# Kernel optimization log

Hardware: AMD Instinct MI355X
Metric: run time of the kernel (lower is better)

Reference implementation:

```python
import jax, jax.numpy as jnp
import numpy as np

NMS_PRE_MAXSIZE = 4096
NMS_POST_MAXSIZE = 512
NMS_THRESH = 0.7


def setup_inputs() -> dict:
    key = jax.random.key(0)
    k1, k2, k3, k4, k5 = jax.random.split(key, 5)
    B, N, C = 4, 32768, 3
    # realistic 3D boxes: (x, y, z, dx, dy, dz, heading)
    xy = jax.random.uniform(k1, (B, N, 2), dtype=jnp.float32) * 70.0
    z = jax.random.uniform(k2, (B, N, 1), dtype=jnp.float32) * 4.0 - 2.0
    sizes = jax.random.uniform(k3, (B, N, 3), dtype=jnp.float32) * 3.0 + 1.0
    heading = jax.random.uniform(k4, (B, N, 1), dtype=jnp.float32) * 6.2832 - 3.1416
    batch_box_preds = jnp.concatenate([xy, z, sizes, heading], axis=-1)  # (B,N,7)
    batch_cls_preds = jax.random.uniform(k5, (B, N, C), dtype=jnp.float32)  # (B,N,3)
    return {"batch_box_preds": batch_box_preds, "batch_cls_preds": batch_cls_preds}


def _nms_single(boxes, scores, labels):
    # boxes (N,7), scores (N,), labels (N,) int32
    top_s, idx = jax.lax.top_k(scores, NMS_PRE_MAXSIZE)   # sort desc, keep pre-maxsize
    b = boxes[idx]                                        # (PRE,7)
    l = labels[idx]
    # BEV axis-aligned IoU (reference surrogate for the rotated-BEV CUDA IoU kernel)
    x, y, dx, dy = b[:, 0], b[:, 1], b[:, 3], b[:, 4]
    x1, x2 = x - 0.5 * dx, x + 0.5 * dx
    y1, y2 = y - 0.5 * dy, y + 0.5 * dy
    area = dx * dy
    ix = jnp.maximum(0.0, jnp.minimum(x2[:, None], x2[None, :]) - jnp.maximum(x1[:, None], x1[None, :]))
    iy = jnp.maximum(0.0, jnp.minimum(y2[:, None], y2[None, :]) - jnp.maximum(y1[:, None], y1[None, :]))
    inter = ix * iy
    iou = jax.lax.stop_gradient(inter / (area[:, None] + area[None, :] - inter + 1e-6))

    ar = jnp.arange(NMS_PRE_MAXSIZE)

    def body(i, keep):
        sup = (iou[i] > NMS_THRESH) & (ar > i) & keep[i]
        return keep & ~sup

    keep = jax.lax.fori_loop(0, NMS_PRE_MAXSIZE, body, jnp.ones(NMS_PRE_MAXSIZE, bool))

    # pack first NMS_POST_MAXSIZE kept boxes into fixed-size zero-padded outputs
    rank = jnp.cumsum(keep) - 1
    valid = keep & (rank < NMS_POST_MAXSIZE)
    pos = jnp.where(valid, rank, NMS_POST_MAXSIZE)  # invalid -> scratch row
    rois = jnp.zeros((NMS_POST_MAXSIZE + 1, 7), b.dtype).at[pos].set(b)[:NMS_POST_MAXSIZE]
    sc = jnp.zeros((NMS_POST_MAXSIZE + 1,), top_s.dtype).at[pos].set(top_s)[:NMS_POST_MAXSIZE]
    lb = jnp.zeros((NMS_POST_MAXSIZE + 1,), jnp.int32).at[pos].set(l)[:NMS_POST_MAXSIZE]
    return rois, sc, lb


def reference(batch_box_preds, batch_cls_preds):
    # per-box max score / argmax class (torch.max(cls_preds, dim=1) per sample)
    roi_scores_all = jnp.max(batch_cls_preds, axis=-1)                 # (B,N)
    roi_labels_all = jnp.argmax(batch_cls_preds, axis=-1).astype(jnp.int32)
    rois, roi_scores, roi_labels = jax.vmap(_nms_single)(batch_box_preds, roi_scores_all, roi_labels_all)
    return rois, roi_scores, roi_labels + 1  # labels shifted by +1 as in proposal_layer
```

## Files before the change

### kernel.cpp

```cpp
#include <hip/hip_runtime.h>
#include <stdint.h>

#define BB 4
#define NN 32768
#define PRE 4096
#define POST 512
#define NMS_TH 0.7f
#define MIDCAP 8192
#define NWAVE 16
#define KCAP 576

typedef unsigned long long u64;
typedef unsigned int u32;

__device__ __forceinline__ u32 orderable(float f) {
  u32 u = __float_as_uint(f);
  return (u & 0x80000000u) ? ~u : (u | 0x80000000u);
}
__device__ __forceinline__ float unorderable(u32 o) {
  u32 u = (o & 0x80000000u) ? (o & 0x7fffffffu) : ~o;
  return __uint_as_float(u);
}
__device__ __forceinline__ u32 bucket_of(float s) {
  u32 v = (u32)(s * 2147483648.0f);
  u32 bk = v >> 20;
  return bk > 2047u ? 2047u : bk;
}
__device__ __forceinline__ u64 readlane64(u64 v, int l) {
  u32 lo = (u32)__builtin_amdgcn_readlane((int)(u32)v, l);
  u32 hi = (u32)__builtin_amdgcn_readlane((int)(u32)(v >> 32), l);
  return ((u64)hi << 32) | lo;
}
__device__ __forceinline__ bool iou_fast(float4 a, float aa, float4 b, float ba, float& mm) {
  float ix = fminf(a.z, b.z) - fmaxf(a.x, b.x); ix = fmaxf(0.0f, ix);
  float iy = fminf(a.w, b.w) - fmaxf(a.y, b.y); iy = fmaxf(0.0f, iy);
  float inter = ix * iy;
  float denom = ((aa + ba) - inter) + 1e-6f;
  float t = 0.7f * denom;
  mm = fminf(mm, fabsf(inter - t) - 2e-5f * t);
  return inter > t;
}
__device__ __forceinline__ bool iou_exact(float4 a, float aa, float4 b, float ba) {
  float ix = fminf(a.z, b.z) - fmaxf(a.x, b.x); ix = fmaxf(0.0f, ix);
  float iy = fminf(a.w, b.w) - fmaxf(a.y, b.y); iy = fmaxf(0.0f, iy);
  float inter = ix * iy;
  float denom = ((aa + ba) - inter) + 1e-6f;
  return (inter / denom) > NMS_TH;
}

__global__ __launch_bounds__(1024, 1) void nms_all_kernel(
    const float* __restrict__ boxes, const float* __restrict__ cls,
    u64* __restrict__ keysG, int* __restrict__ labelsG,
    u64* __restrict__ selG, u64* __restrict__ midG,
    float4* __restrict__ Pg, float* __restrict__ ARg,
    float* __restrict__ topBox, float* __restrict__ topS, int* __restrict__ topL,
    float* __restrict__ out) {
  __shared__ u32 sfx[2048];
  __shared__ u32 cursor[2048];
  __shared__ float4 keptP[KCAP];
  __shared__ float keptAR[KCAP];
  __shared__ u64 dLDS[64];
  __shared__ u64 kwLDS[64];
  __shared__ u32 supArr[64];
  __shared__ u32 midCnt, Tsh, C1sh, knSh;

  int b = blockIdx.x;
  int tid = threadIdx.x;
  int wv = tid >> 6, lane = tid & 63;

  if (tid == 0) { midCnt = 0; knSh = 0; }
  if (tid < 64) kwLDS[tid] = 0;
  for (int t = tid; t < 2048; t += 1024) sfx[t] = 0;
  __syncthreads();

  u64* keysB = keysG + (size_t)b * NN;
  int* labsB = labelsG + (size_t)b * NN;
  const float* clsB = cls + (size_t)b * NN * 3;
  for (int c = 0; c < 8; ++c) {
    int t4 = tid + c * 1024;
    const float4* c4 = (const float4*)(clsB + (size_t)t4 * 12);
    float4 va = c4[0], vb = c4[1], vc = c4[2];
    float v[12] = {va.x, va.y, va.z, va.w, vb.x, vb.y, vb.z, vb.w, vc.x, vc.y, vc.z, vc.w};
    u64 ks[4]; int ls[4];
#pragma unroll
    for (int p = 0; p < 4; ++p) {
      float s = v[3 * p]; int l = 0;
      if (v[3 * p + 1] > s) { s = v[3 * p + 1]; l = 1; }
      if (v[3 * p + 2] > s) { s = v[3 * p + 2]; l = 2; }
      int n = t4 * 4 + p;
      ks[p] = ((u64)orderable(s) << 32) | (u32)(~(u32)n);
      ls[p] = l;
      atomicAdd(&sfx[bucket_of(s)], 1u);
    }
    *(ulonglong2*)(keysB + t4 * 4) = make_ulonglong2(ks[0], ks[1]);
    *(ulonglong2*)(keysB + t4 * 4 + 2) = make_ulonglong2(ks[2], ks[3]);
    *(int4*)(labsB + t4 * 4) = make_int4(ls[0], ls[1], ls[2], ls[3]);
  }
  __syncthreads();

  for (int d = 1; d < 2048; d <<= 1) {
    int t0 = tid, t1 = tid + 1024;
    u32 v0 = (t0 + d < 2048) ? sfx[t0 + d] : 0;
    u32 v1 = (t1 + d < 2048) ? sfx[t1 + d] : 0;
    __syncthreads();
    sfx[t0] += v0; sfx[t1] += v1;
    __syncthreads();
  }
#pragma unroll
  for (int i = 0; i < 2; ++i) {
    int t = tid + i * 1024;
    u32 above = (t + 1 < 2048) ? sfx[t + 1] : 0;
    cursor[t] = above;
    if (above < PRE && sfx[t] >= PRE) { Tsh = (u32)t; C1sh = above; }
  }
  __syncthreads();
  u32 T = Tsh, C1 = C1sh;

  u64* selB = selG + ((size_t)b << 12);
  u64* midB = midG + (size_t)b * MIDCAP;
  for (int c = 0; c < 8; ++c) {
    int t4 = tid + c * 1024;
    ulonglong2 k01 = *(const ulonglong2*)(keysB + t4 * 4);
    ulonglong2 k23 = *(const ulonglong2*)(keysB + t4 * 4 + 2);
    u64 kk[4] = {k01.x, k01.y, k23.x, k23.y};
#pragma unroll
    for (int p = 0; p < 4; ++p) {
      u64 key = kk[p];
      u32 bk = bucket_of(unorderable((u32)(key >> 32)));
      if (bk > T) {
        u32 q = atomicAdd(&cursor[bk], 1u);
        selB[q] = key;
      } else if (bk == T) {
        u32 q = atomicAdd(&midCnt, 1u);
        if (q < MIDCAP) midB[q] = key;
      }
    }
  }
  __syncthreads();

  for (int t = (int)T + wv; t < 2048; t += NWAVE) {
    if (t == (int)T) {
      int need = PRE - (int)C1;
      int M = (int)midCnt; if (M > MIDCAP) M = MIDCAP;
      for (int r = 0; r < need; ++r) {
        u64 best = 0; int bi = -1;
        for (int q = lane; q < M; q += 64) {
          u64 v = midB[q];
          if (v > best) { best = v; bi = q; }
        }
#pragma unroll
        for (int d = 32; d > 0; d >>= 1) {
          u64 ob = __shfl_xor(best, d, 64);
          int oi = __shfl_xor(bi, d, 64);
          if (ob > best) { best = ob; bi = oi; }
        }
        if (lane == 0) selB[C1 + r] = best;
        if (bi >= 0 && lane == (bi & 63)) midB[bi] = 0;
      }
      continue;
    }
    u32 start = (t < 2047) ? sfx[t + 1] : 0u;
    u32 end = sfx[t];
    int n = (int)(end - start);
    if (n <= 1) continue;
    if (n <= 64) {
      u64 v = (lane < n) ? selB[start + lane] : 0ULL;
#pragma unroll
      for (int k = 2; k <= 64; k <<= 1) {
#pragma unroll
        for (int j = k >> 1; j > 0; j >>= 1) {
          u64 o = __shfl_xor(v, j, 64);
          bool up = ((lane & k) == 0);
          bool first = ((lane & j) == 0);
          u64 mx = v > o ? v : o, mn = v > o ? o : v;
          v = (first == up) ? mx : mn;
        }
      }
      if (lane < n) selB[start + lane] = v;
    } else {
      for (int r = 0; r < n - 1; ++r) {
        u64 best = 0; int bi = -1;
        for (int q = r + lane; q < n; q += 64) {
          u64 v = selB[start + q];
          if (v > best) { best = v; bi = q; }
        }
#pragma unroll
        for (int d = 32; d > 0; d >>= 1) {
          u64 ob = __shfl_xor(best, d, 64);
          int oi = __shfl_xor(bi, d, 64);
          if (ob > best) { best = ob; bi = oi; }
        }
        if (lane == 0) {
          u64 tmp = selB[start + r];
          selB[start + r] = best;
          selB[start + bi] = tmp;
        }
      }
    }
  }
  __syncthreads();

  for (int c = 0; c < 4; ++c) {
    int pos = tid + c * 1024;
    u64 key = selB[pos];
    u32 n = ~(u32)key;
    size_t src = (size_t)b * NN + n;
    const float* bx = boxes + src * 7;
    float x = bx[0], y = bx[1], dx = bx[3], dy = bx[4];
    size_t gidx = ((size_t)b << 12) + pos;
    float* tb = topBox + gidx * 7;
#pragma unroll
    for (int cc = 0; cc < 7; ++cc) tb[cc] = bx[cc];
    float4 p;
    p.x = x - 0.5f * dx; p.z = x + 0.5f * dx;
    p.y = y - 0.5f * dy; p.w = y + 0.5f * dy;
    Pg[gidx] = p;
    ARg[gidx] = dx * dy;
    topS[gidx] = unorderable((u32)(key >> 32));
    topL[gidx] = labelsG[src];
  }
  __syncthreads();

  size_t pb = (size_t)b << 12;
  for (int g = 0; g < 64; ++g) {
    int kn0 = (int)knSh;
    int cj = g * 64 + 4 * wv + (lane >> 4);
    float4 cp = Pg[pb + cj];
    float car = ARg[pb + cj];
    bool hit = false; float mm = 1.0f;
    for (int m = (lane & 15); m < kn0; m += 16) {
      hit |= iou_fast(keptP[m], keptAR[m], cp, car, mm);
    }
    if (__any(mm <= 0.0f)) {
      hit = false;
      for (int m = (lane & 15); m < kn0; m += 16)
        hit |= iou_exact(keptP[m], keptAR[m], cp, car);
    }
    u64 bal = __ballot(hit);
    int q = lane >> 4;
    if ((lane & 15) == 0)
      supArr[4 * wv + q] = (((bal >> (16 * q)) & 0xFFFFull) != 0ull) ? 1u : 0u;
    float4 cq = Pg[pb + g * 64 + lane];
    float cqa = ARg[pb + g * 64 + lane];
#pragma unroll
    for (int rr = 0; rr < 4; ++rr) {
      int rj = g * 64 + 4 * wv + rr;
      float4 rp = Pg[pb + rj];
      float rar = ARg[pb + rj];
      float mm2 = 1.0f;
      bool sup = iou_fast(rp, rar, cq, cqa, mm2);
      if (__any(mm2 <= 0.0f)) sup = iou_exact(rp, rar, cq, cqa);
      u64 dw = __ballot(sup);
      if (lane == 0) dLDS[4 * wv + rr] = dw;
    }
    __syncthreads();
    if (wv == 0) {
      u64 d_cur = dLDS[lane];
      u64 sup_word = __ballot(supArr[lane] != 0u);
      u64 aboveMask = ~((2ULL << lane) - 1ULL);
      u64 rem = __ballot((d_cur & aboveMask) != 0ULL);
      if (rem) {
        do {
          int k = __ffsll((long long)rem) - 1;
          rem &= rem - 1;
          if (!((sup_word >> k) & 1ULL))
            sup_word |= readlane64(d_cur, k) & ~((2ULL << k) - 1ULL);
        } while (rem);
      }
      u64 keep = ~sup_word;
      int cnt = __popcll(keep);
      int rank = (int)__popcll(keep & ((1ULL << lane) - 1ULL));
      if ((keep >> lane) & 1ULL) {
        int bi = g * 64 + lane;
        keptP[kn0 + rank] = Pg[pb + bi];
        keptAR[kn0 + rank] = ARg[pb + bi];
      }
      if (lane == 0) { kwLDS[g] = keep; knSh = (u32)(kn0 + cnt); }
    }
    __syncthreads();
    if (knSh >= POST) break;
  }

  if (wv != 0) return;
  u64 kw = kwLDS[lane];
  int cnt = __popcll(kw);
  int pfx = cnt;
#pragma unroll
  for (int d = 1; d < 64; d <<= 1) {
    int up = __shfl_up(pfx, d, 64);
    if (lane >= d) pfx += up;
  }
  int total = __shfl(pfx, 63, 64);
  int pos = pfx - cnt;
  float* outR = out;
  float* outS = out + BB * POST * 7;
  float* outL = outS + BB * POST;
  while (kw) {
    int t = __ffsll((long long)kw) - 1;
    kw &= kw - 1;
    if (pos < POST) {
      int i = (lane << 6) + t;
      int gdx = (b << 9) + pos;
      const float* tb = topBox + (pb + i) * 7;
#pragma unroll
      for (int c = 0; c < 7; ++c) outR[(size_t)gdx * 7 + c] = tb[c];
      outS[gdx] = topS[pb + i];
      outL[gdx] = (float)(topL[pb + i] + 1);
    }
    ++pos;
  }
  int fin = total < POST ? total : POST;
  for (int s = fin + lane; s < POST; s += 64) {
    int gdx = (b << 9) + s;
#pragma unroll
    for (int c = 0; c < 7; ++c) outR[(size_t)gdx * 7 + c] = 0.0f;
    outS[gdx] = 0.0f;
    outL[gdx] = 1.0f;
  }
}

extern "C" void kernel_launch(void* const* d_in, const int* in_sizes, int n_in,
                              void* d_out, int out_size, void* d_ws, size_t ws_size,
                              hipStream_t stream) {
  const float* boxes = (const float*)d_in[0];
  const float* cls   = (const float*)d_in[1];
  float* out = (float*)d_out;

  char* p = (char*)d_ws;
  auto take = [&](size_t bytes) { char* r = p; p += (bytes + 255) & ~(size_t)255; return (void*)r; };
  u64*   keys    = (u64*)  take((size_t)BB * NN * 8);
  int*   labels  = (int*)  take((size_t)BB * NN * 4);
  u64*   sel     = (u64*)  take((size_t)BB * PRE * 8);
  u64*   mid     = (u64*)  take((size_t)BB * MIDCAP * 8);
  float4* Pg     = (float4*)take((size_t)BB * PRE * 16);
  float* ARg     = (float*)take((size_t)BB * PRE * 4);
  float* topBox  = (float*)take((size_t)BB * PRE * 7 * 4);
  float* topS    = (float*)take((size_t)BB * PRE * 4);
  int*   topL    = (int*)  take((size_t)BB * PRE * 4);

  nms_all_kernel<<<BB, 1024, 0, stream>>>(boxes, cls, keys, labels, sel, mid,
                                          Pg, ARg, topBox, topS, topL, out);
}
```

Baseline: 96.98 us.

## Split pre-NMS selection across eight cooperative blocks per batch with grid syncs

Replaces the one-block-per-batch kernel with a cooperative launch of 8 blocks per batch. Each block scores and histograms one slice. Partial histograms are combined through global memory across grid syncs, and scatter cursors move from shared to global atomics. Per-bucket sorting and the top-box gather are spread over all 128 waves and fused so each wave gathers its own bucket. The sequential NMS still runs on one block per batch, and the change adds three grid-wide barriers and extra global atomics.

Measured after the change: 121.7 us. +25.5%, slower.

```diff
diff --git a/kernel.cpp b/kernel.cpp
--- a/kernel.cpp
+++ b/kernel.cpp
@@ -1,5 +1,8 @@
 #include <hip/hip_runtime.h>
+#include <hip/hip_cooperative_groups.h>
 #include <stdint.h>
+
+namespace cg = cooperative_groups;
 
 #define BB 4
 #define NN 32768
@@ -7,8 +10,9 @@
 #define POST 512
 #define NMS_TH 0.7f
 #define MIDCAP 8192
-#define NWAVE 16
 #define KCAP 576
+#define BPB 8
+#define NBLK (BB * BPB)
 
 typedef unsigned long long u64;
 typedef unsigned int u32;
@@ -48,36 +52,39 @@
   return (inter / denom) > NMS_TH;
 }
 
-__global__ __launch_bounds__(1024, 1) void nms_all_kernel(
+__global__ __launch_bounds__(1024, 1) void nms_coop_kernel(
     const float* __restrict__ boxes, const float* __restrict__ cls,
     u64* __restrict__ keysG, int* __restrict__ labelsG,
     u64* __restrict__ selG, u64* __restrict__ midG,
     float4* __restrict__ Pg, float* __restrict__ ARg,
     float* __restrict__ topBox, float* __restrict__ topS, int* __restrict__ topL,
+    u32* __restrict__ gcur, u32* __restrict__ cnt_mid, u32* __restrict__ histP,
     float* __restrict__ out) {
+  cg::grid_group grid = cg::this_grid();
   __shared__ u32 sfx[2048];
-  __shared__ u32 cursor[2048];
   __shared__ float4 keptP[KCAP];
   __shared__ float keptAR[KCAP];
   __shared__ u64 dLDS[64];
   __shared__ u64 kwLDS[64];
   __shared__ u32 supArr[64];
-  __shared__ u32 midCnt, Tsh, C1sh, knSh;
-
-  int b = blockIdx.x;
+  __shared__ u32 Tsh, C1sh, knSh;
+
   int tid = threadIdx.x;
+  int b = blockIdx.x >> 3, sub = blockIdx.x & 7;
   int wv = tid >> 6, lane = tid & 63;
 
-  if (tid == 0) { midCnt = 0; knSh = 0; }
-  if (tid < 64) kwLDS[tid] = 0;
+  {
+    int zid = blockIdx.x * 1024 + tid;
+    if (zid < BB * 2048) gcur[zid] = 0;
+    if (zid < BB) cnt_mid[zid] = 0;
+  }
   for (int t = tid; t < 2048; t += 1024) sfx[t] = 0;
   __syncthreads();
-
   u64* keysB = keysG + (size_t)b * NN;
   int* labsB = labelsG + (size_t)b * NN;
   const float* clsB = cls + (size_t)b * NN * 3;
-  for (int c = 0; c < 8; ++c) {
-    int t4 = tid + c * 1024;
+  {
+    int t4 = sub * 1024 + tid;
     const float4* c4 = (const float4*)(clsB + (size_t)t4 * 12);
     float4 va = c4[0], vb = c4[1], vc = c4[2];
     float v[12] = {va.x, va.y, va.z, va.w, vb.x, vb.y, vb.z, vb.w, vc.x, vc.y, vc.z, vc.w};
@@ -97,7 +104,16 @@
     *(int4*)(labsB + t4 * 4) = make_int4(ls[0], ls[1], ls[2], ls[3]);
   }
   __syncthreads();
-
+  for (int t = tid; t < 2048; t += 1024) histP[(size_t)blockIdx.x * 2048 + t] = sfx[t];
+  grid.sync();
+
+  for (int t = tid; t < 2048; t += 1024) {
+    u32 s = 0;
+#pragma unroll
+    for (int j = 0; j < BPB; ++j) s += histP[(size_t)(b * BPB + j) * 2048 + t];
+    sfx[t] = s;
+  }
+  __syncthreads();
   for (int d = 1; d < 2048; d <<= 1) {
     int t0 = tid, t1 = tid + 1024;
     u32 v0 = (t0 + d < 2048) ? sfx[t0 + d] : 0;
@@ -110,7 +126,6 @@
   for (int i = 0; i < 2; ++i) {
     int t = tid + i * 1024;
     u32 above = (t + 1 < 2048) ? sfx[t + 1] : 0;
-    cursor[t] = above;
     if (above < PRE && sfx[t] >= PRE) { Tsh = (u32)t; C1sh = above; }
   }
   __syncthreads();
@@ -118,8 +133,8 @@
 
   u64* selB = selG + ((size_t)b << 12);
   u64* midB = midG + (size_t)b * MIDCAP;
-  for (int c = 0; c < 8; ++c) {
-    int t4 = tid + c * 1024;
+  {
+    int t4 = sub * 1024 + tid;
     ulonglong2 k01 = *(const ulonglong2*)(keysB + t4 * 4);
     ulonglong2 k23 = *(const ulonglong2*)(keysB + t4 * 4 + 2);
     u64 kk[4] = {k01.x, k01.y, k23.x, k23.y};
@@ -128,20 +143,24 @@
       u64 key = kk[p];
       u32 bk = bucket_of(unorderable((u32)(key >> 32)));
       if (bk > T) {
-        u32 q = atomicAdd(&cursor[bk], 1u);
+        u32 base = (bk < 2047u) ? sfx[bk + 1] : 0u;
+        u32 q = base + atomicAdd(&gcur[b * 2048 + bk], 1u);
         selB[q] = key;
       } else if (bk == T) {
-        u32 q = atomicAdd(&midCnt, 1u);
+        u32 q = atomicAdd(&cnt_mid[b], 1u);
         if (q < MIDCAP) midB[q] = key;
       }
     }
   }
-  __syncthreads();
-
-  for (int t = (int)T + wv; t < 2048; t += NWAVE) {
-    if (t == (int)T) {
+  grid.sync();
+
+  int gw = sub * 16 + wv;
+  for (int i = gw; (int)T + i < 2048; i += BPB * 16) {
+    int t = (int)T + i;
+    u32 start, end;
+    if (i == 0) {
       int need = PRE - (int)C1;
-      int M = (int)midCnt; if (M > MIDCAP) M = MIDCAP;
+      int M = (int)cnt_mid[b]; if (M > MIDCAP) M = MIDCAP;
       for (int r = 0; r < need; ++r) {
         u64 best = 0; int bi = -1;
         for (int q = lane; q < M; q += 64) {
@@ -157,70 +176,72 @@
         if (lane == 0) selB[C1 + r] = best;
         if (bi >= 0 && lane == (bi & 63)) midB[bi] = 0;
       }
-      continue;
-    }
-    u32 start = (t < 2047) ? sfx[t + 1] : 0u;
-    u32 end = sfx[t];
-    int n = (int)(end - start);
-    if (n <= 1) continue;
-    if (n <= 64) {
-      u64 v = (lane < n) ? selB[start + lane] : 0ULL;
-#pragma unroll
-      for (int k = 2; k <= 64; k <<= 1) {
-#pragma unroll
-        for (int j = k >> 1; j > 0; j >>= 1) {
-          u64 o = __shfl_xor(v, j, 64);
-          bool up = ((lane & k) == 0);
-          bool first = ((lane & j) == 0);
-          u64 mx = v > o ? v : o, mn = v > o ? o : v;
-          v = (first == up) ? mx : mn;
+      start = C1; end = PRE;
+    } else {
+      start = (t < 2047) ? sfx[t + 1] : 0u;
+      end = sfx[t];
+      int n = (int)(end - start);
+      if (n > 64) {
+        for (int r = 0; r < n - 1; ++r) {
+          u64 best = 0; int bi = -1;
+          for (int q = r + lane; q < n; q += 64) {
+            u64 v = selB[start + q];
+            if (v > best) { best = v; bi = q; }
+          }
+#pragma unroll
+          for (int d = 32; d > 0; d >>= 1) {
+            u64 ob = __shfl_xor(best, d, 64);
+            int oi = __shfl_xor(bi, d, 64);
+            if (ob > best) { best = ob; bi = oi; }
+          }
+          if (lane == 0) {
+            u64 tmp = selB[start + r];
+            selB[start + r] = best;
+            selB[start + bi] = tmp;
+          }
         }
-      }
-      if (lane < n) selB[start + lane] = v;
-    } else {
-      for (int r = 0; r < n - 1; ++r) {
-        u64 best = 0; int bi = -1;
-        for (int q = r + lane; q < n; q += 64) {
-          u64 v = selB[start + q];
-          if (v > best) { best = v; bi = q; }
+      } else if (n > 1) {
+        u64 v = (lane < n) ? selB[start + lane] : 0ULL;
+#pragma unroll
+        for (int k = 2; k <= 64; k <<= 1) {
+#pragma unroll
+          for (int j = k >> 1; j > 0; j >>= 1) {
+            u64 o = __shfl_xor(v, j, 64);
+            bool up = ((lane & k) == 0);
+            bool first = ((lane & j) == 0);
+            u64 mx = v > o ? v : o, mn = v > o ? o : v;
+            v = (first == up) ? mx : mn;
+          }
         }
-#pragma unroll
-        for (int d = 32; d > 0; d >>= 1) {
-          u64 ob = __shfl_xor(best, d, 64);
-          int oi = __shfl_xor(bi, d, 64);
-          if (ob > best) { best = ob; bi = oi; }
-        }
-        if (lane == 0) {
-          u64 tmp = selB[start + r];
-          selB[start + r] = best;
-          selB[start + bi] = tmp;
-        }
-      }
-    }
-  }
-  __syncthreads();
-
-  for (int c = 0; c < 4; ++c) {
-    int pos = tid + c * 1024;
-    u64 key = selB[pos];
-    u32 n = ~(u32)key;
-    size_t src = (size_t)b * NN + n;
-    const float* bx = boxes + src * 7;
-    float x = bx[0], y = bx[1], dx = bx[3], dy = bx[4];
-    size_t gidx = ((size_t)b << 12) + pos;
-    float* tb = topBox + gidx * 7;
-#pragma unroll
-    for (int cc = 0; cc < 7; ++cc) tb[cc] = bx[cc];
-    float4 p;
-    p.x = x - 0.5f * dx; p.z = x + 0.5f * dx;
-    p.y = y - 0.5f * dy; p.w = y + 0.5f * dy;
-    Pg[gidx] = p;
-    ARg[gidx] = dx * dy;
-    topS[gidx] = unorderable((u32)(key >> 32));
-    topL[gidx] = labelsG[src];
-  }
-  __syncthreads();
-
+        if (lane < n) selB[start + lane] = v;
+      }
+    }
+    __builtin_amdgcn_s_waitcnt(0);
+    for (u32 pos = start + lane; pos < end; pos += 64) {
+      u64 key = selB[pos];
+      u32 n = ~(u32)key;
+      size_t src = (size_t)b * NN + n;
+      const float* bx = boxes + src * 7;
+      float x = bx[0], y = bx[1], dx = bx[3], dy = bx[4];
+      size_t gidx = ((size_t)b << 12) + pos;
+      float* tb = topBox + gidx * 7;
+#pragma unroll
+      for (int cc = 0; cc < 7; ++cc) tb[cc] = bx[cc];
+      float4 p;
+      p.x = x - 0.5f * dx; p.z = x + 0.5f * dx;
+      p.y = y - 0.5f * dy; p.w = y + 0.5f * dy;
+      Pg[gidx] = p;
+      ARg[gidx] = dx * dy;
+      topS[gidx] = unorderable((u32)(key >> 32));
+      topL[gidx] = labelsG[src];
+    }
+  }
+  grid.sync();
+
+  if (sub != 0) return;
+  if (tid == 0) knSh = 0;
+  if (tid < 64) kwLDS[tid] = 0;
+  __syncthreads();
   size_t pb = (size_t)b << 12;
   for (int g = 0; g < 64; ++g) {
     int kn0 = (int)knSh;
@@ -228,9 +249,8 @@
     float4 cp = Pg[pb + cj];
     float car = ARg[pb + cj];
     bool hit = false; float mm = 1.0f;
-    for (int m = (lane & 15); m < kn0; m += 16) {
+    for (int m = (lane & 15); m < kn0; m += 16)
       hit |= iou_fast(keptP[m], keptAR[m], cp, car, mm);
-    }
     if (__any(mm <= 0.0f)) {
       hit = false;
       for (int m = (lane & 15); m < kn0; m += 16)
@@ -337,7 +357,14 @@
   float* topBox  = (float*)take((size_t)BB * PRE * 7 * 4);
   float* topS    = (float*)take((size_t)BB * PRE * 4);
   int*   topL    = (int*)  take((size_t)BB * PRE * 4);
-
-  nms_all_kernel<<<BB, 1024, 0, stream>>>(boxes, cls, keys, labels, sel, mid,
-                                          Pg, ARg, topBox, topS, topL, out);
-}
+  u32*   gcur    = (u32*)  take((size_t)BB * 2048 * 4);
+  u32*   cnt_mid = (u32*)  take((size_t)BB * 4);
+  u32*   histP   = (u32*)  take((size_t)NBLK * 2048 * 4);
+
+  void* args[] = {(void*)&boxes, (void*)&cls, (void*)&keys, (void*)&labels,
+                  (void*)&sel, (void*)&mid, (void*)&Pg, (void*)&ARg,
+                  (void*)&topBox, (void*)&topS, (void*)&topL,
+                  (void*)&gcur, (void*)&cnt_mid, (void*)&histP, (void*)&out};
+  hipLaunchCooperativeKernel((void*)nms_coop_kernel, dim3(NBLK), dim3(1024),
+                             args, 0, stream);
+}
```
